# Kernel tuning notes

Hardware: AMD Instinct MI355X
Metric: run time of the kernel (lower is better)

Reference implementation:

```python
import jax, jax.numpy as jnp
import numpy as np

B, S, HID, NH = 8, 1024, 1024, 16
DH = HID // NH
ZERO = 1e-8  # undefined repo constant, assumed small epsilon


def setup_inputs() -> dict:
    key = jax.random.key(0)
    ks = jax.random.split(key, 14)
    sc = 1.0 / np.sqrt(HID)
    inp = {
        "Q": jax.random.normal(ks[0], (B, S, HID), jnp.float32),
        "K": jax.random.normal(ks[1], (B, S, HID), jnp.float32),
        "V": jax.random.normal(ks[2], (B, S, HID), jnp.float32),
        "Q_mask": jax.random.randint(ks[3], (B, S), 0, 2).astype(jnp.float32),
        "K_mask": jax.random.randint(ks[4], (B, S), 0, 2).astype(jnp.float32),
        "Wq": jax.random.normal(ks[5], (HID, HID), jnp.float32) * sc,
        "bq": jnp.zeros((HID,), jnp.float32),
        "Wk": jax.random.normal(ks[6], (HID, HID), jnp.float32) * sc,
        "bk": jnp.zeros((HID,), jnp.float32),
        "Wv": jax.random.normal(ks[7], (HID, HID), jnp.float32) * sc,
        "bv": jnp.zeros((HID,), jnp.float32),
        "Wo": jax.random.normal(ks[8], (HID, HID), jnp.float32) * sc,
        "bo": jnp.zeros((HID,), jnp.float32),
    }
    return inp


def _heads(x):  # [B,S,HID] -> [B,NH,S,DH]
    b, s, _ = x.shape
    return x.reshape(b, s, NH, DH).transpose(0, 2, 1, 3)


def reference(Q, K, V, Q_mask, K_mask, Wq, bq, Wk, bk, Wv, bv, Wo, bo):
    q = _heads(Q @ Wq.T + bq)
    k = _heads(K @ Wk.T + bk)
    v = _heads(V @ Wv.T + bv)
    # NOTE: original divides by head_size**(-0.5) == multiply by sqrt(DH)
    scores = jnp.einsum("bhqd,bhkd->bhqk", q, k) / (DH ** (-0.5))
    mask = Q_mask[:, :, None] * K_mask[:, None, :]  # [B,Sq,Sk]
    probs = jax.nn.softmax(scores, axis=-1)
    probs = jnp.where(mask[:, None, :, :] == 0, 0.0, probs)
    probs = probs / jnp.sum(probs + ZERO, axis=-1, keepdims=True)
    ctx = jnp.einsum("bhqk,bhkd->bqhd", probs, v).reshape(Q.shape[0], Q.shape[1], HID)
    return ctx @ Wo.T + bo
```

## Files before the change

kernel.cpp:

```cpp
#include <hip/hip_runtime.h>
#include <math.h>

constexpr int Bc   = 8;
constexpr int Sc   = 1024;
constexpr int HIDc = 1024;
constexpr int NHc  = 16;
constexpr int DHc  = 64;
constexpr int Mc   = Bc * Sc;
constexpr int Kc2  = 1024;
constexpr float SCALE    = 8.0f;
constexpr float EPS_TERM = 1024.0f * 1e-8f;

typedef short s16x8 __attribute__((ext_vector_type(8)));
typedef float f32x4 __attribute__((ext_vector_type(4)));

__device__ __forceinline__ ushort f2bf(float f) {
  unsigned u = __float_as_uint(f);
  u += 0x7FFFu + ((u >> 16) & 1u);
  return (ushort)(u >> 16);
}
__device__ __forceinline__ float bf2f(ushort h) {
  return __uint_as_float(((unsigned)h) << 16);
}

__device__ __forceinline__ void gl_lds16(const ushort* g, ushort* l) {
  __builtin_amdgcn_global_load_lds(
      (const __attribute__((address_space(1))) void*)g,
      (__attribute__((address_space(3))) void*)l, 16, 0, 0);
}

__global__ __launch_bounds__(256) void cvt_split(const float4* __restrict__ x,
    ushort4* __restrict__ hi, ushort4* __restrict__ lo, int n4)
{
  const int i = blockIdx.x * 256 + threadIdx.x;
  if (i >= n4) return;
  const float4 v = x[i];
  ushort4 h, l;
  h.x = f2bf(v.x); l.x = f2bf(v.x - bf2f(h.x));
  h.y = f2bf(v.y); l.y = f2bf(v.y - bf2f(h.y));
  h.z = f2bf(v.z); l.z = f2bf(v.z - bf2f(h.z));
  h.w = f2bf(v.w); l.w = f2bf(v.w - bf2f(h.w));
  hi[i] = h; lo[i] = l;
}

__global__ __launch_bounds__(256) void cvt_one(const float4* __restrict__ x,
    ushort4* __restrict__ hi, int n4)
{
  const int i = blockIdx.x * 256 + threadIdx.x;
  if (i >= n4) return;
  const float4 v = x[i];
  ushort4 h;
  h.x = f2bf(v.x); h.y = f2bf(v.y); h.z = f2bf(v.z); h.w = f2bf(v.w);
  hi[i] = h;
}

template<bool SPLIT3>
__global__ __launch_bounds__(256, 3) void mfma_gemm(
    const ushort* __restrict__ Ah_g, const ushort* __restrict__ Al_g,
    const ushort* __restrict__ Bh_g, const ushort* __restrict__ Bl_g,
    const float* __restrict__ bias,
    void* __restrict__ C, void* __restrict__ C2, int mode)
{
  __shared__ ushort AhL[4096];
  __shared__ ushort BhL[4096];
  __shared__ ushort AlL[SPLIT3 ? 4096 : 8];
  __shared__ ushort BlL[SPLIT3 ? 4096 : 8];

  const int t    = threadIdx.x;
  const int w    = t >> 6;
  const int ln   = t & 63;
  const int col  = ln & 15;
  const int quad = ln >> 4;
  const int wm   = w >> 1, wn = w & 1;
  const int m0   = blockIdx.y * 128;
  const int n0   = blockIdx.x * 128;

  f32x4 acc[4][4] = {};

  const int sA = w * 128;

  for (int k0 = 0; k0 < Kc2; k0 += 32) {
    __syncthreads();
#pragma unroll
    for (int j = 0; j < 2; j++) {
      const int s = sA + j * 64 + ln;
      const int r = s & 127, c = s >> 7;
      const size_t goA = (size_t)(m0 + r) * Kc2 + k0 + c * 8;
      const size_t goB = (size_t)(n0 + r) * Kc2 + k0 + c * 8;
      ushort* la = &AhL[(size_t)(sA + j * 64) * 8];
      ushort* lb = &BhL[(size_t)(sA + j * 64) * 8];
      gl_lds16(Ah_g + goA, la);
      gl_lds16(Bh_g + goB, lb);
      if constexpr (SPLIT3) {
        gl_lds16(Al_g + goA, &AlL[(size_t)(sA + j * 64) * 8]);
        gl_lds16(Bl_g + goB, &BlL[(size_t)(sA + j * 64) * 8]);
      }
    }
    __syncthreads();

    s16x8 a_h[4], b_h[4], a_l[4], b_l[4];
#pragma unroll
    for (int i = 0; i < 4; i++) {
      const int ai = (quad * 128 + wm * 64 + i * 16 + col) * 8;
      const int bi = (quad * 128 + wn * 64 + i * 16 + col) * 8;
      a_h[i] = *(const s16x8*)&AhL[ai];
      b_h[i] = *(const s16x8*)&BhL[bi];
      if constexpr (SPLIT3) {
        a_l[i] = *(const s16x8*)&AlL[ai];
        b_l[i] = *(const s16x8*)&BlL[bi];
      }
    }
#pragma unroll
    for (int i = 0; i < 4; i++)
#pragma unroll
      for (int jj = 0; jj < 4; jj++) {
        acc[i][jj] = __builtin_amdgcn_mfma_f32_16x16x32_bf16(a_h[i], b_h[jj], acc[i][jj], 0, 0, 0);
        if constexpr (SPLIT3) {
          acc[i][jj] = __builtin_amdgcn_mfma_f32_16x16x32_bf16(a_h[i], b_l[jj], acc[i][jj], 0, 0, 0);
          acc[i][jj] = __builtin_amdgcn_mfma_f32_16x16x32_bf16(a_l[i], b_h[jj], acc[i][jj], 0, 0, 0);
        }
      }
  }

  const int mb = m0 + wm * 64;
  const int nb = n0 + wn * 64;
#pragma unroll
  for (int i = 0; i < 4; i++)
#pragma unroll
    for (int jj = 0; jj < 4; jj++) {
      const int n  = nb + jj * 16 + col;
      const float bv = bias[n];
#pragma unroll
      for (int r = 0; r < 4; r++) {
        const int m   = mb + i * 16 + quad * 4 + r;
        const float v = acc[i][jj][r] + bv;
        if (mode == 0) {
          ((float*)C)[(size_t)m * HIDc + n] = v;
        } else {
          const int b_ = m >> 10, s = m & (Sc - 1);
          const int h_ = n >> 6,  d = n & (DHc - 1);
          if (mode == 1) {
            const size_t off = (((size_t)b_ * NHc + h_) * Sc + s) * DHc + d;
            const ushort hb = f2bf(v);
            ((ushort*)C)[off]  = hb;
            ((ushort*)C2)[off] = f2bf(v - bf2f(hb));
          } else {
            const size_t off = (((size_t)b_ * NHc + h_) * DHc + d) * Sc + s;
            ((ushort*)C)[off] = f2bf(v);
          }
        }
      }
    }
}

constexpr int TK  = 64;
constexpr int LDK = 72;

__global__ __launch_bounds__(256, 3) void attn_mfma(
    const ushort* __restrict__ qhi, const ushort* __restrict__ qlo,
    const ushort* __restrict__ khi, const ushort* __restrict__ klo,
    const ushort* __restrict__ vt,  const float* __restrict__ Qm,
    const float* __restrict__ Km,   ushort* __restrict__ ctx)
{
  __shared__ ushort KhiL[64 * LDK];
  __shared__ ushort KloL[64 * LDK];
  __shared__ ushort VtL [64 * LDK];
  __shared__ ushort PmL [64 * LDK];
  __shared__ float  kmL[TK];

  const int t    = threadIdx.x;
  const int w    = t >> 6;
  const int ln   = t & 63;
  const int col  = ln & 15;
  const int quad = ln >> 4;

  const int blk = blockIdx.x;
  const int qt  = blk & 15;
  const int bh  = blk >> 4;
  const int b   = bh >> 4;
  const int h   = bh & 15;

  const int qbase = qt * 64 + w * 16;
  const size_t headoff = (size_t)bh * Sc * DHc;

  s16x8 qh0, qh1, ql0, ql1;
  {
    const size_t ro = headoff + (size_t)(qbase + col) * DHc + quad * 8;
    qh0 = *(const s16x8*)(qhi + ro);
    qh1 = *(const s16x8*)(qhi + ro + 32);
    ql0 = *(const s16x8*)(qlo + ro);
    ql1 = *(const s16x8*)(qlo + ro + 32);
  }

  f32x4 O[4] = {{0,0,0,0},{0,0,0,0},{0,0,0,0},{0,0,0,0}};
  float mrow[4] = {-INFINITY, -INFINITY, -INFINITY, -INFINITY};
  float Zr[4]   = {0,0,0,0};
  float Zmr[4]  = {0,0,0,0};

  for (int k0 = 0; k0 < Sc; k0 += TK) {
    __syncthreads();
    for (int i = t; i < 512; i += 256) {
      const int rr = i >> 3, cc = (i & 7) * 8;
      *(s16x8*)&KhiL[rr * LDK + cc] = *(const s16x8*)(khi + headoff + (size_t)(k0 + rr) * DHc + cc);
      *(s16x8*)&KloL[rr * LDK + cc] = *(const s16x8*)(klo + headoff + (size_t)(k0 + rr) * DHc + cc);
      *(s16x8*)&VtL [rr * LDK + cc] = *(const s16x8*)(vt  + headoff + (size_t)rr * Sc + k0 + cc);
    }
    if (t < TK) kmL[t] = Km[b * Sc + k0 + t];
    __syncthreads();

    float s[4][4];
#pragma unroll
    for (int ks = 0; ks < 4; ks++) {
      const ushort* kp = &KhiL[(ks * 16 + col) * LDK];
      const ushort* lp = &KloL[(ks * 16 + col) * LDK];
      const s16x8 kh0 = *(const s16x8*)(kp + quad * 8);
      const s16x8 kh1 = *(const s16x8*)(kp + 32 + quad * 8);
      const s16x8 kl0 = *(const s16x8*)(lp + quad * 8);
      const s16x8 kl1 = *(const s16x8*)(lp + 32 + quad * 8);
      f32x4 acc = {0,0,0,0};
      acc = __builtin_amdgcn_mfma_f32_16x16x32_bf16(qh0, kh0, acc, 0, 0, 0);
      acc = __builtin_amdgcn_mfma_f32_16x16x32_bf16(qh1, kh1, acc, 0, 0, 0);
      acc = __builtin_amdgcn_mfma_f32_16x16x32_bf16(qh0, kl0, acc, 0, 0, 0);
      acc = __builtin_amdgcn_mfma_f32_16x16x32_bf16(qh1, kl1, acc, 0, 0, 0);
      acc = __builtin_amdgcn_mfma_f32_16x16x32_bf16(ql0, kh0, acc, 0, 0, 0);
      acc = __builtin_amdgcn_mfma_f32_16x16x32_bf16(ql1, kh1, acc, 0, 0, 0);
#pragma unroll
      for (int r = 0; r < 4; r++) s[ks][r] = acc[r] * SCALE;
    }

    float kmv[4];
#pragma unroll
    for (int ks = 0; ks < 4; ks++) kmv[ks] = kmL[ks * 16 + col];

    float tmax[4];
#pragma unroll
    for (int r = 0; r < 4; r++)
      tmax[r] = fmaxf(fmaxf(s[0][r], s[1][r]), fmaxf(s[2][r], s[3][r]));
#pragma unroll
    for (int off = 1; off < 16; off <<= 1)
#pragma unroll
      for (int r = 0; r < 4; r++)
        tmax[r] = fmaxf(tmax[r], __shfl_xor(tmax[r], off, 64));

    float alpha[4];
#pragma unroll
    for (int r = 0; r < 4; r++) {
      const float mn = fmaxf(mrow[r], tmax[r]);
      alpha[r] = __expf(mrow[r] - mn);
      mrow[r]  = mn;
    }

    float psum[4] = {0,0,0,0}, pmsum[4] = {0,0,0,0};
#pragma unroll
    for (int ks = 0; ks < 4; ks++)
#pragma unroll
      for (int r = 0; r < 4; r++) {
        const float p  = __expf(s[ks][r] - mrow[r]);
        const float pm = p * kmv[ks];
        psum[r]  += p;
        pmsum[r] += pm;
        s[ks][r]  = pm;
      }
#pragma unroll
    for (int off = 1; off < 16; off <<= 1)
#pragma unroll
      for (int r = 0; r < 4; r++) {
        psum[r]  += __shfl_xor(psum[r],  off, 64);
        pmsum[r] += __shfl_xor(pmsum[r], off, 64);
      }
#pragma unroll
    for (int r = 0; r < 4; r++) {
      Zr[r]  = Zr[r]  * alpha[r] + psum[r];
      Zmr[r] = Zmr[r] * alpha[r] + pmsum[r];
    }

#pragma unroll
    for (int ks = 0; ks < 4; ks++)
#pragma unroll
      for (int r = 0; r < 4; r++)
        PmL[(w * 16 + quad * 4 + r) * LDK + ks * 16 + col] = f2bf(s[ks][r]);
#pragma unroll
    for (int dt = 0; dt < 4; dt++)
#pragma unroll
      for (int r = 0; r < 4; r++)
        O[dt][r] *= alpha[r];

    const ushort* pp = &PmL[(w * 16 + col) * LDK];
    const s16x8 p0 = *(const s16x8*)(pp + quad * 8);
    const s16x8 p1 = *(const s16x8*)(pp + 32 + quad * 8);
#pragma unroll
    for (int dt = 0; dt < 4; dt++) {
      const ushort* vp = &VtL[(dt * 16 + col) * LDK];
      const s16x8 v0 = *(const s16x8*)(vp + quad * 8);
      const s16x8 v1 = *(const s16x8*)(vp + 32 + quad * 8);
      O[dt] = __builtin_amdgcn_mfma_f32_16x16x32_bf16(p0, v0, O[dt], 0, 0, 0);
      O[dt] = __builtin_amdgcn_mfma_f32_16x16x32_bf16(p1, v1, O[dt], 0, 0, 0);
    }
  }

#pragma unroll
  for (int r = 0; r < 4; r++) {
    const int srow = qbase + quad * 4 + r;
    const float qmv  = Qm[b * Sc + srow];
    const float rden = (qmv != 0.0f) ? 1.0f / (Zmr[r] + EPS_TERM * Zr[r]) : 0.0f;
#pragma unroll
    for (int dt = 0; dt < 4; dt++)
      ctx[((size_t)(b * Sc + srow)) * HIDc + h * DHc + dt * 16 + col] = f2bf(O[dt][r] * rden);
  }
}

extern "C" void kernel_launch(void* const* d_in, const int* in_sizes, int n_in,
                              void* d_out, int out_size, void* d_ws, size_t ws_size,
                              hipStream_t stream)
{
  const float* Q  = (const float*)d_in[0];
  const float* K  = (const float*)d_in[1];
  const float* V  = (const float*)d_in[2];
  const float* Qm = (const float*)d_in[3];
  const float* Km = (const float*)d_in[4];
  const float* Wq = (const float*)d_in[5];
  const float* bq = (const float*)d_in[6];
  const float* Wk = (const float*)d_in[7];
  const float* bk = (const float*)d_in[8];
  const float* Wv = (const float*)d_in[9];
  const float* bv = (const float*)d_in[10];
  const float* Wo = (const float*)d_in[11];
  const float* bo = (const float*)d_in[12];
  float* out = (float*)d_out;

  const size_t NEL = (size_t)Mc * HIDc;
  const size_t WEL = (size_t)HIDc * HIDc;

  ushort* Wqh = (ushort*)d_ws;
  ushort* Wql = Wqh + WEL;
  ushort* Wkh = Wql + WEL;
  ushort* Wkl = Wkh + WEL;
  ushort* Wvh = Wkl + WEL;
  ushort* Woh = Wvh + WEL;
  ushort* qhi = Woh + WEL;
  ushort* qlo = qhi + NEL;
  ushort* khi = qlo + NEL;
  ushort* klo = khi + NEL;
  ushort* vt  = klo + NEL;
  ushort* A0  = vt  + NEL;
  ushort* A1  = A0  + NEL;

  const int n4i = (int)(NEL / 4);
  const int n4w = (int)(WEL / 4);

  cvt_split<<<n4w / 256, 256, 0, stream>>>((const float4*)Wq, (ushort4*)Wqh, (ushort4*)Wql, n4w);
  cvt_split<<<n4w / 256, 256, 0, stream>>>((const float4*)Wk, (ushort4*)Wkh, (ushort4*)Wkl, n4w);
  cvt_one  <<<n4w / 256, 256, 0, stream>>>((const float4*)Wv, (ushort4*)Wvh, n4w);
  cvt_one  <<<n4w / 256, 256, 0, stream>>>((const float4*)Wo, (ushort4*)Woh, n4w);

  dim3 gg(HIDc / 128, Mc / 128);

  cvt_split<<<n4i / 256, 256, 0, stream>>>((const float4*)Q, (ushort4*)A0, (ushort4*)A1, n4i);
  mfma_gemm<true><<<gg, 256, 0, stream>>>(A0, A1, Wqh, Wql, bq, qhi, qlo, 1);

  cvt_split<<<n4i / 256, 256, 0, stream>>>((const float4*)K, (ushort4*)A0, (ushort4*)A1, n4i);
  mfma_gemm<true><<<gg, 256, 0, stream>>>(A0, A1, Wkh, Wkl, bk, khi, klo, 1);

  cvt_one<<<n4i / 256, 256, 0, stream>>>((const float4*)V, (ushort4*)A0, n4i);
  mfma_gemm<false><<<gg, 256, 0, stream>>>(A0, nullptr, Wvh, nullptr, bv, vt, nullptr, 2);

  attn_mfma<<<Bc * NHc * (Sc / 64), 256, 0, stream>>>(qhi, qlo, khi, klo, vt, Qm, Km, A1);

  mfma_gemm<false><<<gg, 256, 0, stream>>>(A1, nullptr, Woh, nullptr, bo, out, nullptr, 0);
}
```

Baseline: 584.8 us.

## Fuse weight conversions, pad K/V LDS stride, remap attention blocks per XCD, defer row-sum shuffles

```diff
diff --git a/kernel.cpp b/kernel.cpp
--- a/kernel.cpp
+++ b/kernel.cpp
@@ -52,6 +52,41 @@
   ushort4 h;
   h.x = f2bf(v.x); h.y = f2bf(v.y); h.z = f2bf(v.z); h.w = f2bf(v.w);
   hi[i] = h;
+}
+
+__global__ __launch_bounds__(256) void cvt_weights(
+    const float4* __restrict__ Wq, const float4* __restrict__ Wk,
+    const float4* __restrict__ Wv, const float4* __restrict__ Wo,
+    ushort4* __restrict__ Wqh, ushort4* __restrict__ Wql,
+    ushort4* __restrict__ Wkh, ushort4* __restrict__ Wkl,
+    ushort4* __restrict__ Wvh, ushort4* __restrict__ Woh, int n4w)
+{
+  const int bpseg = n4w / 256;
+  const int seg   = blockIdx.x / bpseg;
+  const int li    = (blockIdx.x - seg * bpseg) * 256 + threadIdx.x;
+  if (li >= n4w) return;
+  if (seg == 0) {
+    const float4 v = Wq[li];
+    ushort4 h, l;
+    h.x = f2bf(v.x); l.x = f2bf(v.x - bf2f(h.x));
+    h.y = f2bf(v.y); l.y = f2bf(v.y - bf2f(h.y));
+    h.z = f2bf(v.z); l.z = f2bf(v.z - bf2f(h.z));
+    h.w = f2bf(v.w); l.w = f2bf(v.w - bf2f(h.w));
+    Wqh[li] = h; Wql[li] = l;
+  } else if (seg == 1) {
+    const float4 v = Wk[li];
+    ushort4 h, l;
+    h.x = f2bf(v.x); l.x = f2bf(v.x - bf2f(h.x));
+    h.y = f2bf(v.y); l.y = f2bf(v.y - bf2f(h.y));
+    h.z = f2bf(v.z); l.z = f2bf(v.z - bf2f(h.z));
+    h.w = f2bf(v.w); l.w = f2bf(v.w - bf2f(h.w));
+    Wkh[li] = h; Wkl[li] = l;
+  } else {
+    const float4 v = (seg == 2) ? Wv[li] : Wo[li];
+    ushort4 h;
+    h.x = f2bf(v.x); h.y = f2bf(v.y); h.z = f2bf(v.z); h.w = f2bf(v.w);
+    if (seg == 2) Wvh[li] = h; else Woh[li] = h;
+  }
 }
 
 template<bool SPLIT3>
@@ -154,7 +189,8 @@
 }
 
 constexpr int TK  = 64;
-constexpr int LDK = 72;
+constexpr int LDK = 80;
+constexpr int LDP = 72;
 
 __global__ __launch_bounds__(256, 3) void attn_mfma(
     const ushort* __restrict__ qhi, const ushort* __restrict__ qlo,
@@ -165,7 +201,7 @@
   __shared__ ushort KhiL[64 * LDK];
   __shared__ ushort KloL[64 * LDK];
   __shared__ ushort VtL [64 * LDK];
-  __shared__ ushort PmL [64 * LDK];
+  __shared__ ushort PmL [64 * LDP];
   __shared__ float  kmL[TK];
 
   const int t    = threadIdx.x;
@@ -174,9 +210,11 @@
   const int col  = ln & 15;
   const int quad = ln >> 4;
 
-  const int blk = blockIdx.x;
-  const int qt  = blk & 15;
-  const int bh  = blk >> 4;
+  const int id  = blockIdx.x;
+  const int xcd = id & 7;
+  const int j   = id >> 3;
+  const int bh  = xcd * 16 + (j >> 4);
+  const int qt  = j & 15;
   const int b   = bh >> 4;
   const int h   = bh & 15;
 
@@ -250,42 +288,33 @@
       mrow[r]  = mn;
     }
 
-    float psum[4] = {0,0,0,0}, pmsum[4] = {0,0,0,0};
-#pragma unroll
-    for (int ks = 0; ks < 4; ks++)
-#pragma unroll
-      for (int r = 0; r < 4; r++) {
+#pragma unroll
+    for (int r = 0; r < 4; r++) {
+      float ps = 0.0f, pms = 0.0f;
+#pragma unroll
+      for (int ks = 0; ks < 4; ks++) {
         const float p  = __expf(s[ks][r] - mrow[r]);
         const float pm = p * kmv[ks];
-        psum[r]  += p;
-        pmsum[r] += pm;
-        s[ks][r]  = pm;
+        ps  += p;
+        pms += pm;
+        s[ks][r] = pm;
       }
-#pragma unroll
-    for (int off = 1; off < 16; off <<= 1)
-#pragma unroll
-      for (int r = 0; r < 4; r++) {
-        psum[r]  += __shfl_xor(psum[r],  off, 64);
-        pmsum[r] += __shfl_xor(pmsum[r], off, 64);
-      }
-#pragma unroll
-    for (int r = 0; r < 4; r++) {
-      Zr[r]  = Zr[r]  * alpha[r] + psum[r];
-      Zmr[r] = Zmr[r] * alpha[r] + pmsum[r];
+      Zr[r]  = Zr[r]  * alpha[r] + ps;
+      Zmr[r] = Zmr[r] * alpha[r] + pms;
     }
 
 #pragma unroll
     for (int ks = 0; ks < 4; ks++)
 #pragma unroll
       for (int r = 0; r < 4; r++)
-        PmL[(w * 16 + quad * 4 + r) * LDK + ks * 16 + col] = f2bf(s[ks][r]);
+        PmL[(w * 16 + quad * 4 + r) * LDP + ks * 16 + col] = f2bf(s[ks][r]);
 #pragma unroll
     for (int dt = 0; dt < 4; dt++)
 #pragma unroll
       for (int r = 0; r < 4; r++)
         O[dt][r] *= alpha[r];
 
-    const ushort* pp = &PmL[(w * 16 + col) * LDK];
+    const ushort* pp = &PmL[(w * 16 + col) * LDP];
     const s16x8 p0 = *(const s16x8*)(pp + quad * 8);
     const s16x8 p1 = *(const s16x8*)(pp + 32 + quad * 8);
 #pragma unroll
@@ -297,6 +326,14 @@
       O[dt] = __builtin_amdgcn_mfma_f32_16x16x32_bf16(p1, v1, O[dt], 0, 0, 0);
     }
   }
+
+#pragma unroll
+  for (int off = 1; off < 16; off <<= 1)
+#pragma unroll
+    for (int r = 0; r < 4; r++) {
+      Zr[r]  += __shfl_xor(Zr[r],  off, 64);
+      Zmr[r] += __shfl_xor(Zmr[r], off, 64);
+    }
 
 #pragma unroll
   for (int r = 0; r < 4; r++) {
@@ -348,10 +385,10 @@
   const int n4i = (int)(NEL / 4);
   const int n4w = (int)(WEL / 4);
 
-  cvt_split<<<n4w / 256, 256, 0, stream>>>((const float4*)Wq, (ushort4*)Wqh, (ushort4*)Wql, n4w);
-  cvt_split<<<n4w / 256, 256, 0, stream>>>((const float4*)Wk, (ushort4*)Wkh, (ushort4*)Wkl, n4w);
-  cvt_one  <<<n4w / 256, 256, 0, stream>>>((const float4*)Wv, (ushort4*)Wvh, n4w);
-  cvt_one  <<<n4w / 256, 256, 0, stream>>>((const float4*)Wo, (ushort4*)Woh, n4w);
+  cvt_weights<<<4 * (n4w / 256), 256, 0, stream>>>(
+      (const float4*)Wq, (const float4*)Wk, (const float4*)Wv, (const float4*)Wo,
+      (ushort4*)Wqh, (ushort4*)Wql, (ushort4*)Wkh, (ushort4*)Wkl,
+      (ushort4*)Wvh, (ushort4*)Woh, n4w);
 
   dim3 gg(HIDc / 128, Mc / 128);
 
```

New measurement: 532.4 us. 9.0% less time.
